# Performance work log

Measured on AMD Instinct MI355X. Metric: run time of the kernel, lower is better.

The kernel has to match this reference:

```python
import jax, jax.numpy as jnp
import numpy as np

NHEADS = 16
HEAD_DIM = 128
HIDDEN = 2048
SOFTCAP = 50.0
ROPE_BASE = 10000.0
SCALE = 256.0 ** (-0.5)  # hardcoded in original, NOT head_dim**-0.5


def _rope_tables(T, D, dtype):
    inv_freq = 1.0 / (ROPE_BASE ** (jnp.arange(0, D, 2, dtype=jnp.float32) / D))
    pos = jnp.arange(T, dtype=jnp.float32)
    freqs = pos[:, None] * inv_freq[None, :]            # [T, D/2]
    emb = jnp.concatenate([freqs, freqs], axis=-1)      # [T, D]
    # broadcast shape [1, 1, T, D] for (B, H, T, D) q/k
    return jnp.cos(emb)[None, None].astype(dtype), jnp.sin(emb)[None, None].astype(dtype)


def _rotate_half(x):
    x1, x2 = x[..., : x.shape[-1] // 2], x[..., x.shape[-1] // 2:]
    return jnp.concatenate([-x2, x1], axis=-1)


def setup_inputs() -> dict:
    key = jax.random.key(0)
    ks = jax.random.split(key, 5)
    B, T = 1, 4096
    X = jax.random.normal(ks[0], (B, T, HIDDEN), dtype=jnp.float32)
    std = 0.02
    Wq = jax.random.normal(ks[1], (HIDDEN, NHEADS * HEAD_DIM), dtype=jnp.float32) * std
    Wk = jax.random.normal(ks[2], (HIDDEN, NHEADS * HEAD_DIM), dtype=jnp.float32) * std
    Wv = jax.random.normal(ks[3], (HIDDEN, NHEADS * HEAD_DIM), dtype=jnp.float32) * std
    Wo = jax.random.normal(ks[4], (NHEADS * HEAD_DIM, HIDDEN), dtype=jnp.float32) * std
    return {"X": X, "Wq": Wq, "Wk": Wk, "Wv": Wv, "Wo": Wo}


def reference(X, Wq, Wk, Wv, Wo):
    B, T, C = X.shape
    H, D = NHEADS, HEAD_DIM
    # QKV projections -> [B, H, T, D]
    q = (X @ Wq).reshape(B, T, H, D).transpose(0, 2, 1, 3)
    k = (X @ Wk).reshape(B, T, H, D).transpose(0, 2, 1, 3)
    v = (X @ Wv).reshape(B, T, H, D).transpose(0, 2, 1, 3)
    # RoPE
    cos, sin = _rope_tables(T, D, X.dtype)
    q = q * cos + _rotate_half(q) * sin
    k = k * cos + _rotate_half(k) * sin
    # attention logits with tanh softcapping
    att = jnp.einsum("bhqd,bhkd->bhqk", q, k) * SCALE
    att = jnp.tanh(att / SOFTCAP) * SOFTCAP
    causal = jnp.tril(jnp.ones((T, T), dtype=bool))[None, None]
    att = jnp.where(causal, att, -jnp.inf)
    att = jax.nn.softmax(att, axis=-1)
    # dropout is identity (train=False)
    y = jnp.einsum("bhqk,bhkd->bhqd", att, v)
    y = y.transpose(0, 2, 1, 3).reshape(B, T, H * D)
    return y @ Wo
```

## Files before the change

kernel.cpp:

```cpp
#include <hip/hip_runtime.h>
#include <stdint.h>

#define T_SEQ 4096
#define HID   2048
#define NH    16
#define HD    128

typedef __attribute__((ext_vector_type(8))) short short8;
typedef __attribute__((ext_vector_type(4))) short short4v;
typedef __attribute__((ext_vector_type(4))) float f32x4;

typedef __attribute__((address_space(1))) void as1_void;
typedef __attribute__((address_space(3))) void as3_void;

__device__ __forceinline__ unsigned short f2bf(float f){
  unsigned u = __builtin_bit_cast(unsigned, f);
  u += 0x7fffu + ((u >> 16) & 1u);
  return (unsigned short)(u >> 16);
}
__device__ __forceinline__ float bf2f(unsigned short b){
  unsigned u = ((unsigned)b) << 16;
  return __builtin_bit_cast(float, u);
}
__device__ __forceinline__ void gll16(const void* g, void* l){
  __builtin_amdgcn_global_load_lds((as1_void*)(uintptr_t)g,
                                   (as3_void*)(unsigned)(uintptr_t)l, 16, 0, 0);
}

#define VM_WAIT(N)  asm volatile("s_waitcnt vmcnt(" #N ")" ::: "memory")
#define LGKM_WAIT0  asm volatile("s_waitcnt lgkmcnt(0)" ::: "memory")
__device__ __forceinline__ void barrier_fence(){
  asm volatile("" ::: "memory");
  __builtin_amdgcn_s_barrier();
  asm volatile("" ::: "memory");
}

__global__ __launch_bounds__(256) void conv_x_k(const float* __restrict__ X,
                                                unsigned short* __restrict__ O){
  int i = (blockIdx.x * 256 + threadIdx.x) * 4;
  float4 v = *(const float4*)(X + i);
  short4v o;
  o[0] = (short)f2bf(v.x); o[1] = (short)f2bf(v.y);
  o[2] = (short)f2bf(v.z); o[3] = (short)f2bf(v.w);
  *(short4v*)(O + i) = o;
}

__global__ __launch_bounds__(256) void conv_wt_k(const float* __restrict__ W0,
                                                 const float* __restrict__ W1,
                                                 const float* __restrict__ W2,
                                                 const float* __restrict__ W3,
                                                 unsigned short* __restrict__ Wt){
  const float* W = (blockIdx.z == 0) ? W0 : (blockIdx.z == 1) ? W1
                   : (blockIdx.z == 2) ? W2 : W3;
  unsigned short* out = Wt + (size_t)blockIdx.z * HID * HID;
  __shared__ float tile[32][33];
  const int x = threadIdx.x;
  const int y = threadIdx.y;
  const int k0 = blockIdx.y * 32, n0 = blockIdx.x * 32;
#pragma unroll
  for (int i = 0; i < 4; ++i){
    int r = y * 4 + i;
    tile[r][x] = W[(size_t)(k0 + r) * HID + n0 + x];
  }
  __syncthreads();
#pragma unroll
  for (int i = 0; i < 4; ++i){
    int r = y * 4 + i;
    out[(size_t)(n0 + r) * HID + k0 + x] = f2bf(tile[x][r]);
  }
}

template<int MODE, int NTOT>
__global__ __launch_bounds__(256, 3) void gemm_bt(
    const unsigned short* __restrict__ A,
    const unsigned short* __restrict__ Bt,
    unsigned short* __restrict__ Qb,
    unsigned short* __restrict__ Kb,
    unsigned short* __restrict__ Vt,
    float* __restrict__ Cf)
{
  constexpr int K = HID;
  __shared__ __align__(16) unsigned short lA[128 * 64];
  __shared__ __align__(16) unsigned short lB[128 * 64];

  const int tid  = threadIdx.x;
  const int wave = tid >> 6;
  const int lane = tid & 63;
  const int qd   = lane >> 4;
  const int mm   = lane & 15;
  const int m7   = mm & 7;
  const int wm   = wave >> 1;
  const int wn   = wave & 1;
  const int bm   = blockIdx.y * 128;
  const int bn   = blockIdx.x * 128;

  const unsigned short* ga[4];
  const unsigned short* gb[4];
  unsigned short* la[4];
  unsigned short* lbp[4];
#pragma unroll
  for (int i = 0; i < 4; ++i){
    int s0   = (wave * 4 + i) * 64;
    int slot = s0 + lane;
    int row  = slot >> 3;
    int kb   = (slot & 7) ^ (row & 7);
    ga[i]  = A  + (size_t)(bm + row) * K + kb * 8;
    gb[i]  = Bt + (size_t)(bn + row) * K + kb * 8;
    la[i]  = lA + s0 * 8;
    lbp[i] = lB + s0 * 8;
  }

  int abase[4], bbase[4];
#pragma unroll
  for (int t = 0; t < 4; ++t){
    abase[t] = (wm * 64 + t * 16 + mm) * 8;
    bbase[t] = (wn * 64 + t * 16 + mm) * 8;
  }

  const f32x4 fzero = {0.f, 0.f, 0.f, 0.f};
  f32x4 acc[4][4];
#pragma unroll
  for (int i = 0; i < 4; ++i)
#pragma unroll
    for (int j = 0; j < 4; ++j) acc[i][j] = fzero;

  for (int k0 = 0; k0 < K; k0 += 64){
    __syncthreads();
#pragma unroll
    for (int i = 0; i < 4; ++i){
      gll16(ga[i] + k0, la[i]);
      gll16(gb[i] + k0, lbp[i]);
    }
    __syncthreads();
#pragma unroll
    for (int ks = 0; ks < 2; ++ks){
      const int co = (ks * 4 + qd) ^ m7;
      short8 af[4], bfv[4];
#pragma unroll
      for (int t = 0; t < 4; ++t) af[t]  = *(const short8*)(lA + (abase[t] + co) * 8);
#pragma unroll
      for (int t = 0; t < 4; ++t) bfv[t] = *(const short8*)(lB + (bbase[t] + co) * 8);
#pragma unroll
      for (int i = 0; i < 4; ++i)
#pragma unroll
        for (int j = 0; j < 4; ++j)
          acc[i][j] = __builtin_amdgcn_mfma_f32_16x16x32_bf16(af[i], bfv[j], acc[i][j], 0, 0, 0);
    }
  }

#pragma unroll
  for (int i = 0; i < 4; ++i){
#pragma unroll
    for (int j = 0; j < 4; ++j){
      const int col = bn + wn * 64 + j * 16 + mm;
#pragma unroll
      for (int r = 0; r < 4; ++r){
        const int row = bm + wm * 64 + i * 16 + qd * 4 + r;
        const float v = acc[i][j][r];
        if (MODE == 0){
          const int sel = col >> 11;
          const int nn  = col & 2047;
          const int h   = nn >> 7;
          const int d   = nn & 127;
          const unsigned short bv = f2bf(v);
          if (sel == 0)      Qb[((size_t)h * T_SEQ + row) * HD + d] = bv;
          else if (sel == 1) Kb[((size_t)h * T_SEQ + row) * HD + d] = bv;
          else               Vt[((size_t)(h * HD + d)) * T_SEQ + row] = bv;
        } else {
          Cf[(size_t)row * NTOT + col] = v;
        }
      }
    }
  }
}

__global__ __launch_bounds__(256) void rope_k(unsigned short* __restrict__ Qb,
                                              unsigned short* __restrict__ Kb){
  const int j = threadIdx.x & 63;
  const int t = blockIdx.x * 4 + (threadIdx.x >> 6);
  const int h = blockIdx.y;
  const float fr = (float)t * __expf(-(float)j * (9.210340371976184f / 64.f));
  const float cs = cosf(fr), sn = sinf(fr);
  const size_t base = ((size_t)h * T_SEQ + t) * HD;
  {
    float x1 = bf2f(Qb[base + j]), x2 = bf2f(Qb[base + j + 64]);
    Qb[base + j]      = f2bf(x1 * cs - x2 * sn);
    Qb[base + j + 64] = f2bf(x2 * cs + x1 * sn);
  }
  {
    float x1 = bf2f(Kb[base + j]), x2 = bf2f(Kb[base + j + 64]);
    Kb[base + j]      = f2bf(x1 * cs - x2 * sn);
    Kb[base + j + 64] = f2bf(x2 * cs + x1 * sn);
  }
}

__global__ __launch_bounds__(256, 2) void attn_k(
    const unsigned short* __restrict__ Qb,
    const unsigned short* __restrict__ Kb,
    const unsigned short* __restrict__ Vt,
    unsigned short* __restrict__ Yb)
{
  __shared__ __align__(16) unsigned char smem[57600];
  unsigned short* lK = (unsigned short*)smem;
  unsigned short* lV = (unsigned short*)(smem + 32768);
  unsigned short (*lP)[32][32] = (unsigned short(*)[32][32])(smem + 49152);
  float* lL = (float*)(smem + 57344);
  float* lO = (float*)smem;

  const int tid  = threadIdx.x;
  const int w    = tid >> 6;
  const int rg   = w >> 1;
  const int kg   = w & 1;
  const int lane = tid & 63;
  const int qd   = lane >> 4;
  const int cc   = lane & 15;
  const int cx   = cc & 7;
  const int r8   = lane >> 3, c7 = lane & 7;

  const int b = blockIdx.x;
  const int h = (b & 7) + 8 * (b >> 8);
  const int pairP = (b >> 3) & 31;

  const int ce  = cc ^ qd;
  const int dlt = (ce & 4) ? -32 : 32;
  const unsigned short* gKbp = Kb + ((size_t)h * T_SEQ + w * 16 + qd) * HD + ce * 8;
  const int cV = c7 ^ r8;
  const unsigned short* gVbp = Vt + ((size_t)h * HD + w * 32 + r8) * T_SEQ + cV * 8;

  const int pc0 = (((cc >> 3)    ) ^ qd) * 8 + (cc & 7);
  const int pc1 = (((cc >> 3) + 2) ^ qd) * 8 + (cc & 7);

  const f32x4 fzero = {0.f, 0.f, 0.f, 0.f};
  const float B0 = 0.09016844006f;
  const float B1 = -4.6962728e-8f;
  const float B2 = 2.9351706e-14f;
  const float CLP = 72.134752f;
  short8 onesv;
#pragma unroll
  for (int j = 0; j < 8; ++j) onesv[j] = (short)0x3F80;

#pragma unroll 1
  for (int half = 0; half < 2; ++half){
    const int tp = half ? (63 - pairP) : pairP;
    const int qrow0 = tp * 64 + rg * 32;
    const int iters = tp + 1;

    {
      unsigned short* dK = lK + w * 2048;
#pragma unroll
      for (int i = 0; i < 4; ++i)
        gll16(gKbp + (size_t)(i * 4) * HD + ((i & 1) ? dlt : 0), dK + i * 512);
      unsigned short* dV = lV + w * 2048;
#pragma unroll
      for (int i = 0; i < 4; ++i)
        gll16(gVbp + (size_t)i * 8 * T_SEQ, dV + i * 512);
    }

    short8 qf[2][4];
#pragma unroll
    for (int mt = 0; mt < 2; ++mt)
#pragma unroll
      for (int ks = 0; ks < 4; ++ks)
        qf[mt][ks] = *(const short8*)(Qb + ((size_t)h * T_SEQ + qrow0 + mt * 16 + cc) * HD + ks * 32 + qd * 8);

    f32x4 o[2][8];
    f32x4 acc_l[2];
#pragma unroll
    for (int mt = 0; mt < 2; ++mt){
#pragma unroll
      for (int dn = 0; dn < 8; ++dn) o[mt][dn] = fzero;
      acc_l[mt] = fzero;
    }

    int curo = 0;
#pragma unroll 1
    for (int it = 0; it < iters; ++it){
      const int k0 = it * 64;

      if (it + 1 < iters){
        const unsigned short* gK = gKbp + (size_t)(k0 + 64) * HD;
        unsigned short* dK = lK + (curo ^ 8192) + w * 2048;
#pragma unroll
        for (int i = 0; i < 4; ++i)
          gll16(gK + (size_t)(i * 4) * HD + ((i & 1) ? dlt : 0), dK + i * 512);
        VM_WAIT(8);
      } else {
        VM_WAIT(4);
      }
      barrier_fence();

      const unsigned short* lKc = lK + curo;

      f32x4 S[2][2];
#pragma unroll
      for (int mt = 0; mt < 2; ++mt)
#pragma unroll
        for (int nt = 0; nt < 2; ++nt) S[mt][nt] = fzero;
      __builtin_amdgcn_s_setprio(1);
#pragma unroll
      for (int nt = 0; nt < 2; ++nt){
        short8 kf[4];
#pragma unroll
        for (int ks = 0; ks < 4; ++ks)
          kf[ks] = *(const short8*)(lKc + ((kg * 32 + nt * 16 + cc) * 16 + ((ks * 4 + qd) ^ cx)) * 8);
#pragma unroll
        for (int mt = 0; mt < 2; ++mt)
#pragma unroll
          for (int ks = 0; ks < 4; ++ks)
            S[mt][nt] = __builtin_amdgcn_mfma_f32_16x16x32_bf16(qf[mt][ks], kf[ks], S[mt][nt], 0, 0, 0);
      }
      __builtin_amdgcn_s_setprio(0);

      const bool domask = (it == iters - 1);
#pragma unroll
      for (int mt = 0; mt < 2; ++mt)
#pragma unroll
        for (int nt = 0; nt < 2; ++nt)
#pragma unroll
          for (int r = 0; r < 4; ++r){
            float s = S[mt][nt][r];
            float w2 = s * s;
            float t = fmaf(w2, B2, B1);
            t = fmaf(w2, t, B0);
            float a = s * t;
            a = __builtin_amdgcn_fmed3f(a, -CLP, CLP);
            float p = __builtin_amdgcn_exp2f(a);
            if (domask){
              int col = k0 + kg * 32 + nt * 16 + cc;
              int row = qrow0 + mt * 16 + qd * 4 + r;
              if (col > row) p = 0.f;
            }
            unsigned u = __builtin_bit_cast(unsigned, p);
            lP[w][mt * 16 + qd * 4 + r][nt ? pc1 : pc0] = (unsigned short)(u >> 16);
          }

      if (it + 1 < iters){
        VM_WAIT(4);
      } else {
        VM_WAIT(0);
      }
      barrier_fence();

      short8 pf[2];
#pragma unroll
      for (int mt = 0; mt < 2; ++mt)
        pf[mt] = *(const short8*)(&lP[w][mt * 16 + cc][(qd ^ (cc >> 2)) * 8]);

      __builtin_amdgcn_s_setprio(1);
#pragma unroll
      for (int dn = 0; dn < 8; ++dn){
        short8 vf = *(const short8*)(lV + ((dn * 16 + cc) * 8 + ((kg * 4 + qd) ^ cx)) * 8);
#pragma unroll
        for (int mt = 0; mt < 2; ++mt)
          o[mt][dn] = __builtin_amdgcn_mfma_f32_16x16x32_bf16(pf[mt], vf, o[mt][dn], 0, 0, 0);
      }
#pragma unroll
      for (int mt = 0; mt < 2; ++mt)
        acc_l[mt] = __builtin_amdgcn_mfma_f32_16x16x32_bf16(pf[mt], onesv, acc_l[mt], 0, 0, 0);
      __builtin_amdgcn_s_setprio(0);

      LGKM_WAIT0;
      barrier_fence();

      if (it + 1 < iters){
        const unsigned short* gV = gVbp + (k0 + 64);
        unsigned short* dV = lV + w * 2048;
#pragma unroll
        for (int i = 0; i < 4; ++i)
          gll16(gV + (size_t)i * 8 * T_SEQ, dV + i * 512);
      }
      curo ^= 8192;
    }

    __syncthreads();
    if (kg == 1){
#pragma unroll
      for (int mt = 0; mt < 2; ++mt){
#pragma unroll
        for (int dn = 0; dn < 8; ++dn)
          *(f32x4*)&lO[(dn * 16 + cc) * 68 + rg * 32 + mt * 16 + qd * 4] = o[mt][dn];
        if (cc == 0){
#pragma unroll
          for (int r = 0; r < 4; ++r)
            lL[rg * 32 + mt * 16 + qd * 4 + r] = acc_l[mt][r];
        }
      }
    }
    __syncthreads();
    if (kg == 0){
#pragma unroll
      for (int mt = 0; mt < 2; ++mt){
        float inv[4];
#pragma unroll
        for (int r = 0; r < 4; ++r){
          float lt = acc_l[mt][r] + lL[rg * 32 + mt * 16 + qd * 4 + r];
          inv[r] = __builtin_amdgcn_rcpf(lt);
        }
#pragma unroll
        for (int dn = 0; dn < 8; ++dn){
          f32x4 oo = o[mt][dn] + *(const f32x4*)&lO[(dn * 16 + cc) * 68 + rg * 32 + mt * 16 + qd * 4];
#pragma unroll
          for (int r = 0; r < 4; ++r){
            int row = qrow0 + mt * 16 + qd * 4 + r;
            Yb[(size_t)row * HID + h * HD + dn * 16 + cc] = f2bf(oo[r] * inv[r]);
          }
        }
      }
    }
    __syncthreads();
  }
}

extern "C" void kernel_launch(void* const* d_in, const int* in_sizes, int n_in,
                              void* d_out, int out_size, void* d_ws, size_t ws_size,
                              hipStream_t stream) {
  const float* X  = (const float*)d_in[0];
  const float* Wq = (const float*)d_in[1];
  const float* Wk = (const float*)d_in[2];
  const float* Wv = (const float*)d_in[3];
  const float* Wo = (const float*)d_in[4];
  float* out = (float*)d_out;

  unsigned short* ws = (unsigned short*)d_ws;
  unsigned short* Xb = ws;
  unsigned short* Wt = ws + (size_t)8  * 1024 * 1024;
  unsigned short* Qb = ws + (size_t)24 * 1024 * 1024;
  unsigned short* Kb = ws + (size_t)32 * 1024 * 1024;
  unsigned short* Vt = ws + (size_t)40 * 1024 * 1024;
  unsigned short* Yb = Xb;

  conv_x_k<<<8192, 256, 0, stream>>>(X, Xb);
  conv_wt_k<<<dim3(64, 64, 4), dim3(32, 8), 0, stream>>>(Wq, Wk, Wv, Wo, Wt);
  gemm_bt<0, 6144><<<dim3(48, 32), 256, 0, stream>>>(Xb, Wt, Qb, Kb, Vt, nullptr);
  rope_k<<<dim3(1024, NH), 256, 0, stream>>>(Qb, Kb);
  attn_k<<<dim3(512), 256, 0, stream>>>(Qb, Kb, Vt, Yb);
  gemm_bt<1, 2048><<<dim3(16, 32), 256, 0, stream>>>(Yb, Wt + (size_t)6144 * 2048,
                                                     nullptr, nullptr, nullptr, out);
}
```

Measured before the change: 441.0 us.

## Single-buffer attention K/V, one tile per block, transpose V epilogue via LDS

The attention kernel drops its double-buffered K and its paired-tile loop. Each block now handles one 64-row query tile, heaviest tiles first, and the grid doubles. The smaller LDS footprint lets the launch bound target 3 blocks per CU, but every iteration now waits on the full K/V load with no prefetch overlap. Separately, the QKV GEMM stages V tiles through LDS to write the transposed Vt with coalesced 16-byte stores instead of scattered 2-byte stores.

```diff
diff --git a/kernel.cpp b/kernel.cpp
--- a/kernel.cpp
+++ b/kernel.cpp
@@ -27,7 +27,7 @@
                                    (as3_void*)(unsigned)(uintptr_t)l, 16, 0, 0);
 }
 
-#define VM_WAIT(N)  asm volatile("s_waitcnt vmcnt(" #N ")" ::: "memory")
+#define VM_WAIT0    asm volatile("s_waitcnt vmcnt(0)" ::: "memory")
 #define LGKM_WAIT0  asm volatile("s_waitcnt lgkmcnt(0)" ::: "memory")
 __device__ __forceinline__ void barrier_fence(){
   asm volatile("" ::: "memory");
@@ -80,8 +80,9 @@
     float* __restrict__ Cf)
 {
   constexpr int K = HID;
-  __shared__ __align__(16) unsigned short lA[128 * 64];
-  __shared__ __align__(16) unsigned short lB[128 * 64];
+  __shared__ __align__(16) unsigned short lAB[16384];
+  unsigned short* lA = lAB;
+  unsigned short* lB = lAB + 8192;
 
   const int tid  = threadIdx.x;
   const int wave = tid >> 6;
@@ -148,6 +149,41 @@
     }
   }
 
+  if (MODE == 0 && bn >= 4096){
+    __syncthreads();
+    unsigned short* lT = lAB;
+#pragma unroll
+    for (int i = 0; i < 4; ++i){
+#pragma unroll
+      for (int j = 0; j < 4; ++j){
+        const int d_l   = wn * 64 + j * 16 + mm;
+        const int chunk = wm * 16 + i * 4 + qd;
+        const int ch    = chunk ^ (d_l & 31);
+        short4v pk;
+#pragma unroll
+        for (int r = 0; r < 4; ++r) pk[r] = (short)f2bf(acc[i][j][r]);
+        *(short4v*)(lT + d_l * 128 + ch * 4) = pk;
+      }
+    }
+    __syncthreads();
+    const int hV = (bn >> 7) - 32;
+    const int dd = tid >> 4;
+    const int tg = tid & 15;
+#pragma unroll
+    for (int p = 0; p < 8; ++p){
+      const int d_l = p * 16 + dd;
+      const int c0  = (tg * 2)     ^ (d_l & 31);
+      const int c1  = (tg * 2 + 1) ^ (d_l & 31);
+      short4v lo = *(const short4v*)(lT + d_l * 128 + c0 * 4);
+      short4v hi = *(const short4v*)(lT + d_l * 128 + c1 * 4);
+      short8 ov;
+      ov[0] = lo[0]; ov[1] = lo[1]; ov[2] = lo[2]; ov[3] = lo[3];
+      ov[4] = hi[0]; ov[5] = hi[1]; ov[6] = hi[2]; ov[7] = hi[3];
+      *(short8*)(Vt + ((size_t)(hV * HD + d_l)) * T_SEQ + bm + tg * 8) = ov;
+    }
+    return;
+  }
+
 #pragma unroll
   for (int i = 0; i < 4; ++i){
 #pragma unroll
@@ -158,14 +194,12 @@
         const int row = bm + wm * 64 + i * 16 + qd * 4 + r;
         const float v = acc[i][j][r];
         if (MODE == 0){
-          const int sel = col >> 11;
           const int nn  = col & 2047;
           const int h   = nn >> 7;
           const int d   = nn & 127;
           const unsigned short bv = f2bf(v);
-          if (sel == 0)      Qb[((size_t)h * T_SEQ + row) * HD + d] = bv;
-          else if (sel == 1) Kb[((size_t)h * T_SEQ + row) * HD + d] = bv;
-          else               Vt[((size_t)(h * HD + d)) * T_SEQ + row] = bv;
+          if (col < 2048)      Qb[((size_t)h * T_SEQ + row) * HD + d] = bv;
+          else                 Kb[((size_t)h * T_SEQ + row) * HD + d] = bv;
         } else {
           Cf[(size_t)row * NTOT + col] = v;
         }
@@ -194,17 +228,17 @@
   }
 }
 
-__global__ __launch_bounds__(256, 2) void attn_k(
+__global__ __launch_bounds__(256, 3) void attn_k(
     const unsigned short* __restrict__ Qb,
     const unsigned short* __restrict__ Kb,
     const unsigned short* __restrict__ Vt,
     unsigned short* __restrict__ Yb)
 {
-  __shared__ __align__(16) unsigned char smem[57600];
+  __shared__ __align__(16) unsigned char smem[41216];
   unsigned short* lK = (unsigned short*)smem;
-  unsigned short* lV = (unsigned short*)(smem + 32768);
-  unsigned short (*lP)[32][32] = (unsigned short(*)[32][32])(smem + 49152);
-  float* lL = (float*)(smem + 57344);
+  unsigned short* lV = (unsigned short*)(smem + 16384);
+  unsigned short (*lP)[32][32] = (unsigned short(*)[32][32])(smem + 32768);
+  float* lL = (float*)(smem + 40960);
   float* lO = (float*)smem;
 
   const int tid  = threadIdx.x;
@@ -217,9 +251,11 @@
   const int cx   = cc & 7;
   const int r8   = lane >> 3, c7 = lane & 7;
 
-  const int b = blockIdx.x;
-  const int h = (b & 7) + 8 * (b >> 8);
-  const int pairP = (b >> 3) & 31;
+  const int b  = blockIdx.x;
+  const int h  = b & 15;
+  const int tp = 63 - (b >> 4);
+  const int qrow0 = tp * 64 + rg * 32;
+  const int iters = tp + 1;
 
   const int ce  = cc ^ qd;
   const int dlt = (ce & 4) ? -32 : 32;
@@ -239,175 +275,151 @@
 #pragma unroll
   for (int j = 0; j < 8; ++j) onesv[j] = (short)0x3F80;
 
+  {
+    unsigned short* dK = lK + w * 2048;
+#pragma unroll
+    for (int i = 0; i < 4; ++i)
+      gll16(gKbp + (size_t)(i * 4) * HD + ((i & 1) ? dlt : 0), dK + i * 512);
+    unsigned short* dV = lV + w * 2048;
+#pragma unroll
+    for (int i = 0; i < 4; ++i)
+      gll16(gVbp + (size_t)i * 8 * T_SEQ, dV + i * 512);
+  }
+
+  short8 qf[2][4];
+#pragma unroll
+  for (int mt = 0; mt < 2; ++mt)
+#pragma unroll
+    for (int ks = 0; ks < 4; ++ks)
+      qf[mt][ks] = *(const short8*)(Qb + ((size_t)h * T_SEQ + qrow0 + mt * 16 + cc) * HD + ks * 32 + qd * 8);
+
+  f32x4 o[2][8];
+  f32x4 acc_l[2];
+#pragma unroll
+  for (int mt = 0; mt < 2; ++mt){
+#pragma unroll
+    for (int dn = 0; dn < 8; ++dn) o[mt][dn] = fzero;
+    acc_l[mt] = fzero;
+  }
+
 #pragma unroll 1
-  for (int half = 0; half < 2; ++half){
-    const int tp = half ? (63 - pairP) : pairP;
-    const int qrow0 = tp * 64 + rg * 32;
-    const int iters = tp + 1;
-
-    {
+  for (int it = 0; it < iters; ++it){
+    const int k0 = it * 64;
+    VM_WAIT0;
+    barrier_fence();
+
+    f32x4 S[2][2];
+#pragma unroll
+    for (int mt = 0; mt < 2; ++mt)
+#pragma unroll
+      for (int nt = 0; nt < 2; ++nt) S[mt][nt] = fzero;
+    __builtin_amdgcn_s_setprio(1);
+#pragma unroll
+    for (int nt = 0; nt < 2; ++nt){
+      short8 kf[4];
+#pragma unroll
+      for (int ks = 0; ks < 4; ++ks)
+        kf[ks] = *(const short8*)(lK + ((kg * 32 + nt * 16 + cc) * 16 + ((ks * 4 + qd) ^ cx)) * 8);
+#pragma unroll
+      for (int mt = 0; mt < 2; ++mt)
+#pragma unroll
+        for (int ks = 0; ks < 4; ++ks)
+          S[mt][nt] = __builtin_amdgcn_mfma_f32_16x16x32_bf16(qf[mt][ks], kf[ks], S[mt][nt], 0, 0, 0);
+    }
+    __builtin_amdgcn_s_setprio(0);
+
+    const bool domask = (it == iters - 1);
+#pragma unroll
+    for (int mt = 0; mt < 2; ++mt)
+#pragma unroll
+      for (int nt = 0; nt < 2; ++nt)
+#pragma unroll
+        for (int r = 0; r < 4; ++r){
+          float s = S[mt][nt][r];
+          float w2 = s * s;
+          float t = fmaf(w2, B2, B1);
+          t = fmaf(w2, t, B0);
+          float a = s * t;
+          a = __builtin_amdgcn_fmed3f(a, -CLP, CLP);
+          float p = __builtin_amdgcn_exp2f(a);
+          if (domask){
+            int col = k0 + kg * 32 + nt * 16 + cc;
+            int row = qrow0 + mt * 16 + qd * 4 + r;
+            if (col > row) p = 0.f;
+          }
+          unsigned u = __builtin_bit_cast(unsigned, p);
+          lP[w][mt * 16 + qd * 4 + r][nt ? pc1 : pc0] = (unsigned short)(u >> 16);
+        }
+
+    short8 pf[2];
+#pragma unroll
+    for (int mt = 0; mt < 2; ++mt)
+      pf[mt] = *(const short8*)(&lP[w][mt * 16 + cc][(qd ^ (cc >> 2)) * 8]);
+
+    __builtin_amdgcn_s_setprio(1);
+#pragma unroll
+    for (int dn = 0; dn < 8; ++dn){
+      short8 vf = *(const short8*)(lV + ((dn * 16 + cc) * 8 + ((kg * 4 + qd) ^ cx)) * 8);
+#pragma unroll
+      for (int mt = 0; mt < 2; ++mt)
+        o[mt][dn] = __builtin_amdgcn_mfma_f32_16x16x32_bf16(pf[mt], vf, o[mt][dn], 0, 0, 0);
+    }
+#pragma unroll
+    for (int mt = 0; mt < 2; ++mt)
+      acc_l[mt] = __builtin_amdgcn_mfma_f32_16x16x32_bf16(pf[mt], onesv, acc_l[mt], 0, 0, 0);
+    __builtin_amdgcn_s_setprio(0);
+
+    LGKM_WAIT0;
+    barrier_fence();
+
+    if (it + 1 < iters){
+      const unsigned short* gK = gKbp + (size_t)(k0 + 64) * HD;
       unsigned short* dK = lK + w * 2048;
 #pragma unroll
       for (int i = 0; i < 4; ++i)
-        gll16(gKbp + (size_t)(i * 4) * HD + ((i & 1) ? dlt : 0), dK + i * 512);
+        gll16(gK + (size_t)(i * 4) * HD + ((i & 1) ? dlt : 0), dK + i * 512);
+      const unsigned short* gV = gVbp + (k0 + 64);
       unsigned short* dV = lV + w * 2048;
 #pragma unroll
       for (int i = 0; i < 4; ++i)
-        gll16(gVbp + (size_t)i * 8 * T_SEQ, dV + i * 512);
-    }
-
-    short8 qf[2][4];
-#pragma unroll
-    for (int mt = 0; mt < 2; ++mt)
-#pragma unroll
-      for (int ks = 0; ks < 4; ++ks)
-        qf[mt][ks] = *(const short8*)(Qb + ((size_t)h * T_SEQ + qrow0 + mt * 16 + cc) * HD + ks * 32 + qd * 8);
-
-    f32x4 o[2][8];
-    f32x4 acc_l[2];
+        gll16(gV + (size_t)i * 8 * T_SEQ, dV + i * 512);
+    }
+  }
+
+  __syncthreads();
+  if (kg == 1){
 #pragma unroll
     for (int mt = 0; mt < 2; ++mt){
 #pragma unroll
-      for (int dn = 0; dn < 8; ++dn) o[mt][dn] = fzero;
-      acc_l[mt] = fzero;
-    }
-
-    int curo = 0;
-#pragma unroll 1
-    for (int it = 0; it < iters; ++it){
-      const int k0 = it * 64;
-
-      if (it + 1 < iters){
-        const unsigned short* gK = gKbp + (size_t)(k0 + 64) * HD;
-        unsigned short* dK = lK + (curo ^ 8192) + w * 2048;
-#pragma unroll
-        for (int i = 0; i < 4; ++i)
-          gll16(gK + (size_t)(i * 4) * HD + ((i & 1) ? dlt : 0), dK + i * 512);
-        VM_WAIT(8);
-      } else {
-        VM_WAIT(4);
+      for (int dn = 0; dn < 8; ++dn)
+        *(f32x4*)&lO[(dn * 16 + cc) * 68 + rg * 32 + mt * 16 + qd * 4] = o[mt][dn];
+      if (cc == 0){
+#pragma unroll
+        for (int r = 0; r < 4; ++r)
+          lL[rg * 32 + mt * 16 + qd * 4 + r] = acc_l[mt][r];
       }
-      barrier_fence();
-
-      const unsigned short* lKc = lK + curo;
-
-      f32x4 S[2][2];
-#pragma unroll
-      for (int mt = 0; mt < 2; ++mt)
-#pragma unroll
-        for (int nt = 0; nt < 2; ++nt) S[mt][nt] = fzero;
-      __builtin_amdgcn_s_setprio(1);
-#pragma unroll
-      for (int nt = 0; nt < 2; ++nt){
-        short8 kf[4];
-#pragma unroll
-        for (int ks = 0; ks < 4; ++ks)
-          kf[ks] = *(const short8*)(lKc + ((kg * 32 + nt * 16 + cc) * 16 + ((ks * 4 + qd) ^ cx)) * 8);
-#pragma unroll
-        for (int mt = 0; mt < 2; ++mt)
-#pragma unroll
-          for (int ks = 0; ks < 4; ++ks)
-            S[mt][nt] = __builtin_amdgcn_mfma_f32_16x16x32_bf16(qf[mt][ks], kf[ks], S[mt][nt], 0, 0, 0);
+    }
+  }
+  __syncthreads();
+  if (kg == 0){
+#pragma unroll
+    for (int mt = 0; mt < 2; ++mt){
+      float inv[4];
+#pragma unroll
+      for (int r = 0; r < 4; ++r){
+        float lt = acc_l[mt][r] + lL[rg * 32 + mt * 16 + qd * 4 + r];
+        inv[r] = __builtin_amdgcn_rcpf(lt);
       }
-      __builtin_amdgcn_s_setprio(0);
-
-      const bool domask = (it == iters - 1);
-#pragma unroll
-      for (int mt = 0; mt < 2; ++mt)
-#pragma unroll
-        for (int nt = 0; nt < 2; ++nt)
-#pragma unroll
-          for (int r = 0; r < 4; ++r){
-            float s = S[mt][nt][r];
-            float w2 = s * s;
-            float t = fmaf(w2, B2, B1);
-            t = fmaf(w2, t, B0);
-            float a = s * t;
-            a = __builtin_amdgcn_fmed3f(a, -CLP, CLP);
-            float p = __builtin_amdgcn_exp2f(a);
-            if (domask){
-              int col = k0 + kg * 32 + nt * 16 + cc;
-              int row = qrow0 + mt * 16 + qd * 4 + r;
-              if (col > row) p = 0.f;
-            }
-            unsigned u = __builtin_bit_cast(unsigned, p);
-            lP[w][mt * 16 + qd * 4 + r][nt ? pc1 : pc0] = (unsigned short)(u >> 16);
-          }
-
-      if (it + 1 < iters){
-        VM_WAIT(4);
-      } else {
-        VM_WAIT(0);
-      }
-      barrier_fence();
-
-      short8 pf[2];
-#pragma unroll
-      for (int mt = 0; mt < 2; ++mt)
-        pf[mt] = *(const short8*)(&lP[w][mt * 16 + cc][(qd ^ (cc >> 2)) * 8]);
-
-      __builtin_amdgcn_s_setprio(1);
 #pragma unroll
       for (int dn = 0; dn < 8; ++dn){
-        short8 vf = *(const short8*)(lV + ((dn * 16 + cc) * 8 + ((kg * 4 + qd) ^ cx)) * 8);
-#pragma unroll
-        for (int mt = 0; mt < 2; ++mt)
-          o[mt][dn] = __builtin_amdgcn_mfma_f32_16x16x32_bf16(pf[mt], vf, o[mt][dn], 0, 0, 0);
-      }
-#pragma unroll
-      for (int mt = 0; mt < 2; ++mt)
-        acc_l[mt] = __builtin_amdgcn_mfma_f32_16x16x32_bf16(pf[mt], onesv, acc_l[mt], 0, 0, 0);
-      __builtin_amdgcn_s_setprio(0);
-
-      LGKM_WAIT0;
-      barrier_fence();
-
-      if (it + 1 < iters){
-        const unsigned short* gV = gVbp + (k0 + 64);
-        unsigned short* dV = lV + w * 2048;
-#pragma unroll
-        for (int i = 0; i < 4; ++i)
-          gll16(gV + (size_t)i * 8 * T_SEQ, dV + i * 512);
-      }
-      curo ^= 8192;
-    }
-
-    __syncthreads();
-    if (kg == 1){
-#pragma unroll
-      for (int mt = 0; mt < 2; ++mt){
-#pragma unroll
-        for (int dn = 0; dn < 8; ++dn)
-          *(f32x4*)&lO[(dn * 16 + cc) * 68 + rg * 32 + mt * 16 + qd * 4] = o[mt][dn];
-        if (cc == 0){
-#pragma unroll
-          for (int r = 0; r < 4; ++r)
-            lL[rg * 32 + mt * 16 + qd * 4 + r] = acc_l[mt][r];
+        f32x4 oo = o[mt][dn] + *(const f32x4*)&lO[(dn * 16 + cc) * 68 + rg * 32 + mt * 16 + qd * 4];
+#pragma unroll
+        for (int r = 0; r < 4; ++r){
+          int row = qrow0 + mt * 16 + qd * 4 + r;
+          Yb[(size_t)row * HID + h * HD + dn * 16 + cc] = f2bf(oo[r] * inv[r]);
         }
       }
     }
-    __syncthreads();
-    if (kg == 0){
-#pragma unroll
-      for (int mt = 0; mt < 2; ++mt){
-        float inv[4];
-#pragma unroll
-        for (int r = 0; r < 4; ++r){
-          float lt = acc_l[mt][r] + lL[rg * 32 + mt * 16 + qd * 4 + r];
-          inv[r] = __builtin_amdgcn_rcpf(lt);
-        }
-#pragma unroll
-        for (int dn = 0; dn < 8; ++dn){
-          f32x4 oo = o[mt][dn] + *(const f32x4*)&lO[(dn * 16 + cc) * 68 + rg * 32 + mt * 16 + qd * 4];
-#pragma unroll
-          for (int r = 0; r < 4; ++r){
-            int row = qrow0 + mt * 16 + qd * 4 + r;
-            Yb[(size_t)row * HID + h * HD + dn * 16 + cc] = f2bf(oo[r] * inv[r]);
-          }
-        }
-      }
-    }
-    __syncthreads();
   }
 }
 
@@ -433,7 +445,7 @@
   conv_wt_k<<<dim3(64, 64, 4), dim3(32, 8), 0, stream>>>(Wq, Wk, Wv, Wo, Wt);
   gemm_bt<0, 6144><<<dim3(48, 32), 256, 0, stream>>>(Xb, Wt, Qb, Kb, Vt, nullptr);
   rope_k<<<dim3(1024, NH), 256, 0, stream>>>(Qb, Kb);
-  attn_k<<<dim3(512), 256, 0, stream>>>(Qb, Kb, Vt, Yb);
+  attn_k<<<dim3(1024), 256, 0, stream>>>(Qb, Kb, Vt, Yb);
   gemm_bt<1, 2048><<<dim3(16, 32), 256, 0, stream>>>(Yb, Wt + (size_t)6144 * 2048,
                                                      nullptr, nullptr, nullptr, out);
 }
```

Measured after the change: 425.7 us. 1.04x faster.
